# Kernel optimization log

Hardware: AMD Instinct MI355X
Metric: run time of the kernel (lower is better)

## Reference

```python
import jax, jax.numpy as jnp
import numpy as np

N_NODES = 100000
N_EDGES = 1600000
D_FEAT = 32
K = 5


def _spmm(edge_row, edge_col, edge_vals, feat):
    # y[i] = sum_{e: row[e]==i} vals[e] * feat[col[e]]  -- sparse A @ feat
    msgs = edge_vals[:, None] * feat[edge_col]  # [E, d]
    return jax.ops.segment_sum(msgs, edge_row, num_segments=N_NODES)


def setup_inputs() -> dict:
    key = jax.random.key(0)
    k1, k2, k3, k4, k5 = jax.random.split(key, 5)
    feat = jax.random.normal(k1, (N_NODES, D_FEAT), dtype=jnp.float32)
    # approximate D^{-1/2} A D^{-1/2} magnitudes: ~1/avg_degree so spectrum stays bounded
    edge_vals = jax.random.uniform(k2, (N_EDGES,), dtype=jnp.float32) * (1.0 / 16.0)
    theta = jnp.asarray([0.5, 0.4, 0.3, 0.2, 0.1], dtype=jnp.float32)
    edge_row = jax.random.randint(k3, (N_EDGES,), 0, N_NODES, dtype=jnp.int32)
    edge_col = jax.random.randint(k4, (N_EDGES,), 0, N_NODES, dtype=jnp.int32)
    return {"feat": feat, "edge_vals": edge_vals, "theta": theta,
            "edge_row": edge_row, "edge_col": edge_col}


def reference(feat, edge_vals, theta, edge_row, edge_col):
    # h = theta[0]*feat; for k>=1: feat = feat - A@feat; h += theta[k]*feat
    h = theta[0] * feat
    for k in range(1, K):
        feat = feat - _spmm(edge_row, edge_col, edge_vals, feat)
        h = h + theta[k] * feat
    return h
```

## Files before the change

### kernel.cpp

```cpp
#include <hip/hip_runtime.h>

#define N_NODES 100000
#define N_EDGES 1600000
#define D_FEAT 32
#define KPOLY 5

#define NWIN 512
#define RPW  ((N_NODES + NWIN - 1) / NWIN)
#define WPAD 16
#define CAP  4096

#define VAL_SCALE 524288.0f
#define VAL_INV   (1.0f / 524288.0f)

#define EB_BS  256
#define EB_EPT 16
#define EB_EPB (EB_BS * EB_EPT)
#define EB_NB  ((N_EDGES + EB_EPB - 1) / EB_EPB)

__device__ __forceinline__ unsigned short f2bf(float f) {
    unsigned u = __float_as_uint(f);
    unsigned r = u + 0x7fffu + ((u >> 16) & 1u);
    return (unsigned short)(r >> 16);
}
__device__ __forceinline__ float bfl(unsigned u) { return __uint_as_float(u << 16); }
__device__ __forceinline__ float bfh(unsigned u) { return __uint_as_float(u & 0xffff0000u); }


__global__ __launch_bounds__(NWIN) void cursor_kernel(int* __restrict__ win_cursor) {
    win_cursor[threadIdx.x * WPAD] = threadIdx.x * CAP;
}


__global__ __launch_bounds__(EB_BS) void bucket_kernel(const int* __restrict__ row,
                                                       const int* __restrict__ col,
                                                       const float* __restrict__ vals,
                                                       int* __restrict__ win_cursor,
                                                       uint2* __restrict__ pile,
                                                       const float* __restrict__ feat,
                                                       unsigned short* __restrict__ feat16,
                                                       int n4) {
    __shared__ int wcnt[NWIN];
    __shared__ int lbase[NWIN];
    __shared__ int wbase[NWIN];
    __shared__ int ps[EB_BS];
    __shared__ uint2 stage[EB_EPB];
    int t = threadIdx.x;
    for (int i = t; i < NWIN; i += EB_BS) wcnt[i] = 0;
    __syncthreads();

    int base = blockIdx.x * EB_EPB;
    unsigned pk_[EB_EPT];
    int wr_[EB_EPT];
#pragma unroll
    for (int i = 0; i < EB_EPT; ++i) {
        int e = base + i * EB_BS + t;
        if (e < N_EDGES) {
            int r = row[e];
            int w = r / RPW;
            unsigned fx = (unsigned)__float2int_rn(vals[e] * VAL_SCALE);
            if (fx > 0x7FFFu) fx = 0x7FFFu;
            pk_[i] = ((unsigned)col[e] << 15) | fx;
            wr_[i] = (w << 8) | (r - w * RPW);
            atomicAdd(&wcnt[w], 1);
        } else wr_[i] = -1;
    }
    __syncthreads();

    int c0 = wcnt[2 * t], c1 = wcnt[2 * t + 1];
    ps[t] = c0 + c1;
    __syncthreads();
    for (int off = 1; off < EB_BS; off <<= 1) {
        int u = (t >= off) ? ps[t - off] : 0;
        __syncthreads();
        ps[t] += u;
        __syncthreads();
    }
    int pex = ps[t] - (c0 + c1);
    lbase[2 * t]     = pex;
    lbase[2 * t + 1] = pex + c0;
    __syncthreads();

    for (int i = t; i < NWIN; i += EB_BS) {
        int cw = wcnt[i];
        wbase[i] = cw ? atomicAdd(&win_cursor[i * WPAD], cw) : 0;
    }
    __syncthreads();
    for (int i = t; i < NWIN; i += EB_BS) wcnt[i] = lbase[i];
    __syncthreads();

#pragma unroll
    for (int i = 0; i < EB_EPT; ++i) {
        if (wr_[i] < 0) continue;
        int w = wr_[i] >> 8;
        int loc = atomicAdd(&wcnt[w], 1);
        stage[loc] = make_uint2(pk_[i], (unsigned)wr_[i]);
    }
    __syncthreads();

    int nedge = N_EDGES - base; if (nedge > EB_EPB) nedge = EB_EPB;
    for (int i = t; i < nedge; i += EB_BS) {
        uint2 ed = stage[i];
        int w = ed.y >> 8;
        int pos = wbase[w] + (i - lbase[w]);
        pile[pos] = make_uint2(ed.x, ed.y & 0xFFu);
    }

    for (int i = blockIdx.x * EB_BS + t; i < n4; i += EB_NB * EB_BS) {
        float4 f = reinterpret_cast<const float4*>(feat)[i];
        ushort4 o;
        o.x = f2bf(f.x); o.y = f2bf(f.y); o.z = f2bf(f.z); o.w = f2bf(f.w);
        reinterpret_cast<ushort4*>(feat16)[i] = o;
    }
}

__global__ __launch_bounds__(256) void finesort_kernel(const uint2* __restrict__ pile,
                                                       const int* __restrict__ win_cursor,
                                                       unsigned int* __restrict__ cvout,
                                                       int2* __restrict__ row_rng) {
    __shared__ int cnt[256];
    __shared__ int incl[256];
    __shared__ int cur[256];
    int w = blockIdx.x, t = threadIdx.x;
    int rbeg = w * RPW;
    int rcnt = N_NODES - rbeg;
    if (rcnt > RPW) rcnt = RPW;
    if (rcnt < 0) rcnt = 0;
    int pbeg = w * CAP;
    int pend = win_cursor[w * WPAD];
    cnt[t] = 0;
    __syncthreads();
    for (int i = pbeg + t; i < pend; i += 256) atomicAdd(&cnt[pile[i].y], 1);
    __syncthreads();
    int v = cnt[t];
    incl[t] = v;
    __syncthreads();
    for (int off = 1; off < 256; off <<= 1) {
        int u = (t >= off) ? incl[t - off] : 0;
        __syncthreads();
        incl[t] += u;
        __syncthreads();
    }
    int ex = incl[t] - v;
    if (t < rcnt) {
        cur[t] = ex;
        row_rng[rbeg + t] = make_int2(pbeg + ex, pbeg + ex + v);
    }
    __syncthreads();
    for (int i = pbeg + t; i < pend; i += 256) {
        uint2 ed = pile[i];
        int pos = atomicAdd(&cur[ed.y], 1);
        cvout[pbeg + pos] = ed.x;
    }
}


#define GATH(qq, pp) \
    uint4 qq = *(reinterpret_cast<const uint4*>(gsrc + (size_t)((pp) >> 15) * D_FEAT) + c)
#define ACC(qq, vv) \
    a0 += (vv) * bfl(qq.x); a1 += (vv) * bfh(qq.x); a2 += (vv) * bfl(qq.y); a3 += (vv) * bfh(qq.y); \
    a4 += (vv) * bfl(qq.z); a5 += (vv) * bfh(qq.z); a6 += (vv) * bfl(qq.w); a7 += (vv) * bfh(qq.w)

__global__ __launch_bounds__(256) void spmm_kernel(const int2* __restrict__ row_rng,
                               const unsigned int* __restrict__ cv,
                               const unsigned short* __restrict__ gsrc,
                               unsigned short* __restrict__ g_out,
                               const unsigned short* __restrict__ f16,
                               const unsigned short* __restrict__ t1,
                               const unsigned short* __restrict__ t2,
                               const float* __restrict__ theta,
                               float* __restrict__ h,
                               int last) {
    int tid = blockIdx.x * blockDim.x + threadIdx.x;
    int r = tid >> 2;
    int c = tid & 3;
    if (r >= N_NODES) return;
    int2 rng = row_rng[r];
    int e = rng.x, end = rng.y;
    float a0=0.f,a1=0.f,a2=0.f,a3=0.f,a4=0.f,a5=0.f,a6=0.f,a7=0.f;

    for (; e + 8 <= end; e += 8) {
        unsigned p0 = cv[e + 0], p1 = cv[e + 1], p2 = cv[e + 2], p3 = cv[e + 3];
        unsigned p4 = cv[e + 4], p5 = cv[e + 5], p6 = cv[e + 6], p7 = cv[e + 7];
        GATH(q0, p0); GATH(q1, p1); GATH(q2, p2); GATH(q3, p3);
        GATH(q4, p4); GATH(q5, p5); GATH(q6, p6); GATH(q7, p7);
        float v0 = (float)(p0 & 0x7FFFu) * VAL_INV;
        float v1 = (float)(p1 & 0x7FFFu) * VAL_INV;
        float v2 = (float)(p2 & 0x7FFFu) * VAL_INV;
        float v3 = (float)(p3 & 0x7FFFu) * VAL_INV;
        float v4 = (float)(p4 & 0x7FFFu) * VAL_INV;
        float v5 = (float)(p5 & 0x7FFFu) * VAL_INV;
        float v6 = (float)(p6 & 0x7FFFu) * VAL_INV;
        float v7 = (float)(p7 & 0x7FFFu) * VAL_INV;
        ACC(q0, v0); ACC(q1, v1); ACC(q2, v2); ACC(q3, v3);
        ACC(q4, v4); ACC(q5, v5); ACC(q6, v6); ACC(q7, v7);
    }
    for (; e + 4 <= end; e += 4) {
        unsigned p0 = cv[e + 0], p1 = cv[e + 1], p2 = cv[e + 2], p3 = cv[e + 3];
        GATH(q0, p0); GATH(q1, p1); GATH(q2, p2); GATH(q3, p3);
        float v0 = (float)(p0 & 0x7FFFu) * VAL_INV;
        float v1 = (float)(p1 & 0x7FFFu) * VAL_INV;
        float v2 = (float)(p2 & 0x7FFFu) * VAL_INV;
        float v3 = (float)(p3 & 0x7FFFu) * VAL_INV;
        ACC(q0, v0); ACC(q1, v1); ACC(q2, v2); ACC(q3, v3);
    }
    for (; e < end; ++e) {
        unsigned p = cv[e];
        float v = (float)(p & 0x7FFFu) * VAL_INV;
        GATH(q, p);
        ACC(q, v);
    }

    size_t base = (size_t)r * D_FEAT + c * 8;
    uint4 qi = *reinterpret_cast<const uint4*>(gsrc + base);
    float c0=bfl(qi.x), c1=bfh(qi.x), c2=bfl(qi.y), c3=bfh(qi.y);
    float c4=bfl(qi.z), c5=bfh(qi.z), c6=bfl(qi.w), c7=bfh(qi.w);
    float n0=c0-a0, n1=c1-a1, n2=c2-a2, n3=c3-a3, n4=c4-a4, n5=c5-a5, n6=c6-a6, n7=c7-a7;

    if (!last) {
        uint4 o;
        o.x = (unsigned)f2bf(n0) | ((unsigned)f2bf(n1) << 16);
        o.y = (unsigned)f2bf(n2) | ((unsigned)f2bf(n3) << 16);
        o.z = (unsigned)f2bf(n4) | ((unsigned)f2bf(n5) << 16);
        o.w = (unsigned)f2bf(n6) | ((unsigned)f2bf(n7) << 16);
        *reinterpret_cast<uint4*>(g_out + base) = o;
    } else {
        float th0 = theta[0], th1 = theta[1], th2 = theta[2], th3 = theta[3], th4 = theta[4];
        uint4 qf = *reinterpret_cast<const uint4*>(f16 + base);
        uint4 q1 = *reinterpret_cast<const uint4*>(t1 + base);
        uint4 q2 = *reinterpret_cast<const uint4*>(t2 + base);
        float4 h0, h1;
        h0.x = th0*bfl(qf.x) + th1*bfl(q1.x) + th2*bfl(q2.x) + th3*c0 + th4*n0;
        h0.y = th0*bfh(qf.x) + th1*bfh(q1.x) + th2*bfh(q2.x) + th3*c1 + th4*n1;
        h0.z = th0*bfl(qf.y) + th1*bfl(q1.y) + th2*bfl(q2.y) + th3*c2 + th4*n2;
        h0.w = th0*bfh(qf.y) + th1*bfh(q1.y) + th2*bfh(q2.y) + th3*c3 + th4*n3;
        h1.x = th0*bfl(qf.z) + th1*bfl(q1.z) + th2*bfl(q2.z) + th3*c4 + th4*n4;
        h1.y = th0*bfh(qf.z) + th1*bfh(q1.z) + th2*bfh(q2.z) + th3*c5 + th4*n5;
        h1.z = th0*bfl(qf.w) + th1*bfl(q1.w) + th2*bfl(q2.w) + th3*c6 + th4*n6;
        h1.w = th0*bfh(qf.w) + th1*bfh(q1.w) + th2*bfh(q2.w) + th3*c7 + th4*n7;
        *reinterpret_cast<float4*>(h + base) = h0;
        *reinterpret_cast<float4*>(h + base + 4) = h1;
    }
}

extern "C" void kernel_launch(void* const* d_in, const int* in_sizes, int n_in,
                              void* d_out, int out_size, void* d_ws, size_t ws_size,
                              hipStream_t stream) {
    const float* feat  = (const float*)d_in[0];
    const float* vals  = (const float*)d_in[1];
    const float* theta = (const float*)d_in[2];
    const int*   row   = (const int*)d_in[3];
    const int*   col   = (const int*)d_in[4];
    float* h = (float*)d_out;

    char* ws = (char*)d_ws;
    size_t off = 0;
    auto alloc = [&](size_t bytes) { void* p = ws + off; off = (off + bytes + 63) & ~(size_t)63; return p; };
    unsigned short* feat16 = (unsigned short*)alloc((size_t)N_NODES * D_FEAT * sizeof(short));
    unsigned short* T1 = (unsigned short*)alloc((size_t)N_NODES * D_FEAT * sizeof(short));
    unsigned short* T2 = (unsigned short*)alloc((size_t)N_NODES * D_FEAT * sizeof(short));
    unsigned short* T3 = (unsigned short*)alloc((size_t)N_NODES * D_FEAT * sizeof(short));
    int2*  row_rng  = (int2*)alloc((size_t)N_NODES * sizeof(int2));
    int*   win_cursor = (int*)alloc((size_t)NWIN * WPAD * sizeof(int));
    uint2* pile     = (uint2*)alloc((size_t)NWIN * CAP * sizeof(uint2));
    unsigned int* cv = (unsigned int*)alloc((size_t)NWIN * CAP * sizeof(unsigned int));

    const int blk = 256;
    const int n4 = N_NODES * D_FEAT / 4;

    cursor_kernel<<<1, NWIN, 0, stream>>>(win_cursor);
    bucket_kernel<<<EB_NB, EB_BS, 0, stream>>>(row, col, vals, win_cursor, pile, feat, feat16, n4);
    finesort_kernel<<<NWIN, 256, 0, stream>>>(pile, win_cursor, cv, row_rng);

    const int sgrid = (N_NODES * 4 + blk - 1) / blk;
    spmm_kernel<<<sgrid, blk, 0, stream>>>(row_rng, cv, feat16, T1, nullptr, nullptr, nullptr, theta, nullptr, 0);
    spmm_kernel<<<sgrid, blk, 0, stream>>>(row_rng, cv, T1, T2, nullptr, nullptr, nullptr, theta, nullptr, 0);
    spmm_kernel<<<sgrid, blk, 0, stream>>>(row_rng, cv, T2, T3, nullptr, nullptr, nullptr, theta, nullptr, 0);
    spmm_kernel<<<sgrid, blk, 0, stream>>>(row_rng, cv, T3, nullptr, feat16, T1, T2, theta, h, 1);
}
```

Before: 141.7 us.

## Fuse per-window fine sort with first SpMM iteration using LDS-resident column list

```diff
diff --git a/kernel.cpp b/kernel.cpp
--- a/kernel.cpp
+++ b/kernel.cpp
@@ -3,7 +3,6 @@
 #define N_NODES 100000
 #define N_EDGES 1600000
 #define D_FEAT 32
-#define KPOLY 5
 
 #define NWIN 512
 #define RPW  ((N_NODES + NWIN - 1) / NWIN)
@@ -27,8 +26,9 @@
 __device__ __forceinline__ float bfh(unsigned u) { return __uint_as_float(u & 0xffff0000u); }
 
 
-__global__ __launch_bounds__(NWIN) void cursor_kernel(int* __restrict__ win_cursor) {
-    win_cursor[threadIdx.x * WPAD] = threadIdx.x * CAP;
+__global__ __launch_bounds__(256) void cursor_kernel(int* __restrict__ win_cursor) {
+    int i = blockIdx.x * 256 + threadIdx.x;
+    if (i < NWIN) win_cursor[i * WPAD] = i * CAP;
 }
 
 
@@ -114,13 +114,24 @@
     }
 }
 
-__global__ __launch_bounds__(256) void finesort_kernel(const uint2* __restrict__ pile,
-                                                       const int* __restrict__ win_cursor,
-                                                       unsigned int* __restrict__ cvout,
-                                                       int2* __restrict__ row_rng) {
+
+#define GATH(qq, pp) \
+    uint4 qq = *(reinterpret_cast<const uint4*>(gsrc + (size_t)((pp) >> 15) * D_FEAT) + c)
+#define ACC(qq, vv) \
+    a0 += (vv) * bfl(qq.x); a1 += (vv) * bfh(qq.x); a2 += (vv) * bfl(qq.y); a3 += (vv) * bfh(qq.y); \
+    a4 += (vv) * bfl(qq.z); a5 += (vv) * bfh(qq.z); a6 += (vv) * bfl(qq.w); a7 += (vv) * bfh(qq.w)
+
+__global__ __launch_bounds__(1024) void finesort_spmm1_kernel(const uint2* __restrict__ pile,
+                               const int* __restrict__ win_cursor,
+                               unsigned int* __restrict__ cvout,
+                               int2* __restrict__ row_rng,
+                               const unsigned short* __restrict__ gsrc,
+                               unsigned short* __restrict__ g_out) {
     __shared__ int cnt[256];
     __shared__ int incl[256];
     __shared__ int cur[256];
+    __shared__ int lbeg[256];
+    __shared__ unsigned cvl[CAP];
     int w = blockIdx.x, t = threadIdx.x;
     int rbeg = w * RPW;
     int rcnt = N_NODES - rbeg;
@@ -128,38 +139,69 @@
     if (rcnt < 0) rcnt = 0;
     int pbeg = w * CAP;
     int pend = win_cursor[w * WPAD];
-    cnt[t] = 0;
-    __syncthreads();
-    for (int i = pbeg + t; i < pend; i += 256) atomicAdd(&cnt[pile[i].y], 1);
-    __syncthreads();
-    int v = cnt[t];
-    incl[t] = v;
+    int n = pend - pbeg;
+    if (t < 256) cnt[t] = 0;
+    __syncthreads();
+    for (int i = pbeg + t; i < pend; i += 1024) atomicAdd(&cnt[pile[i].y], 1);
+    __syncthreads();
+    int v = 0;
+    if (t < 256) { v = cnt[t]; incl[t] = v; }
     __syncthreads();
     for (int off = 1; off < 256; off <<= 1) {
-        int u = (t >= off) ? incl[t - off] : 0;
+        int u = (t < 256 && t >= off) ? incl[t - off] : 0;
         __syncthreads();
-        incl[t] += u;
+        if (t < 256) incl[t] += u;
         __syncthreads();
     }
-    int ex = incl[t] - v;
-    if (t < rcnt) {
+    if (t < 256) {
+        int ex = incl[t] - v;
         cur[t] = ex;
-        row_rng[rbeg + t] = make_int2(pbeg + ex, pbeg + ex + v);
-    }
-    __syncthreads();
-    for (int i = pbeg + t; i < pend; i += 256) {
+        lbeg[t] = ex;
+        if (t < rcnt) row_rng[rbeg + t] = make_int2(pbeg + ex, pbeg + ex + v);
+    }
+    __syncthreads();
+    for (int i = pbeg + t; i < pend; i += 1024) {
         uint2 ed = pile[i];
         int pos = atomicAdd(&cur[ed.y], 1);
+        cvl[pos] = ed.x;
         cvout[pbeg + pos] = ed.x;
     }
-}
-
-
-#define GATH(qq, pp) \
-    uint4 qq = *(reinterpret_cast<const uint4*>(gsrc + (size_t)((pp) >> 15) * D_FEAT) + c)
-#define ACC(qq, vv) \
-    a0 += (vv) * bfl(qq.x); a1 += (vv) * bfh(qq.x); a2 += (vv) * bfl(qq.y); a3 += (vv) * bfh(qq.y); \
-    a4 += (vv) * bfl(qq.z); a5 += (vv) * bfh(qq.z); a6 += (vv) * bfl(qq.w); a7 += (vv) * bfh(qq.w)
+    __syncthreads();
+
+    int ntask = rcnt * 4;
+    if (t < ntask) {
+        int lr = t >> 2, c = t & 3;
+        int e = lbeg[lr];
+        int end = incl[lr];
+        float a0=0.f,a1=0.f,a2=0.f,a3=0.f,a4=0.f,a5=0.f,a6=0.f,a7=0.f;
+        for (; e + 4 <= end; e += 4) {
+            unsigned p0 = cvl[e + 0], p1 = cvl[e + 1], p2 = cvl[e + 2], p3 = cvl[e + 3];
+            GATH(q0, p0); GATH(q1, p1); GATH(q2, p2); GATH(q3, p3);
+            float v0 = (float)(p0 & 0x7FFFu) * VAL_INV;
+            float v1 = (float)(p1 & 0x7FFFu) * VAL_INV;
+            float v2 = (float)(p2 & 0x7FFFu) * VAL_INV;
+            float v3 = (float)(p3 & 0x7FFFu) * VAL_INV;
+            ACC(q0, v0); ACC(q1, v1); ACC(q2, v2); ACC(q3, v3);
+        }
+        for (; e < end; ++e) {
+            unsigned p = cvl[e];
+            float vv = (float)(p & 0x7FFFu) * VAL_INV;
+            GATH(q, p);
+            ACC(q, vv);
+        }
+        size_t base = (size_t)(rbeg + lr) * D_FEAT + c * 8;
+        uint4 qi = *reinterpret_cast<const uint4*>(gsrc + base);
+        float c0=bfl(qi.x), c1=bfh(qi.x), c2=bfl(qi.y), c3=bfh(qi.y);
+        float c4=bfl(qi.z), c5=bfh(qi.z), c6=bfl(qi.w), c7=bfh(qi.w);
+        uint4 o;
+        o.x = (unsigned)f2bf(c0 - a0) | ((unsigned)f2bf(c1 - a1) << 16);
+        o.y = (unsigned)f2bf(c2 - a2) | ((unsigned)f2bf(c3 - a3) << 16);
+        o.z = (unsigned)f2bf(c4 - a4) | ((unsigned)f2bf(c5 - a5) << 16);
+        o.w = (unsigned)f2bf(c6 - a6) | ((unsigned)f2bf(c7 - a7) << 16);
+        *reinterpret_cast<uint4*>(g_out + base) = o;
+    }
+}
+
 
 __global__ __launch_bounds__(256) void spmm_kernel(const int2* __restrict__ row_rng,
                                const unsigned int* __restrict__ cv,
@@ -268,12 +310,11 @@
     const int blk = 256;
     const int n4 = N_NODES * D_FEAT / 4;
 
-    cursor_kernel<<<1, NWIN, 0, stream>>>(win_cursor);
+    cursor_kernel<<<(NWIN + 255) / 256, 256, 0, stream>>>(win_cursor);
     bucket_kernel<<<EB_NB, EB_BS, 0, stream>>>(row, col, vals, win_cursor, pile, feat, feat16, n4);
-    finesort_kernel<<<NWIN, 256, 0, stream>>>(pile, win_cursor, cv, row_rng);
+    finesort_spmm1_kernel<<<NWIN, 1024, 0, stream>>>(pile, win_cursor, cv, row_rng, feat16, T1);
 
     const int sgrid = (N_NODES * 4 + blk - 1) / blk;
-    spmm_kernel<<<sgrid, blk, 0, stream>>>(row_rng, cv, feat16, T1, nullptr, nullptr, nullptr, theta, nullptr, 0);
     spmm_kernel<<<sgrid, blk, 0, stream>>>(row_rng, cv, T1, T2, nullptr, nullptr, nullptr, theta, nullptr, 0);
     spmm_kernel<<<sgrid, blk, 0, stream>>>(row_rng, cv, T2, T3, nullptr, nullptr, nullptr, theta, nullptr, 0);
     spmm_kernel<<<sgrid, blk, 0, stream>>>(row_rng, cv, T3, nullptr, feat16, T1, T2, theta, h, 1);
```

Result: faster. 133.8 us (-5.6%).
